# Kernel tuning notes

Measured on AMD Instinct MI355X. Metric: run time of the kernel, lower is better.

## Reference

```python
import jax, jax.numpy as jnp
import numpy as np

N_ELEM = 10   # len(EnvPara.ELEMENTS)
N_ATOMS = 100000
N_DIM = 256


def setup_inputs() -> dict:
    key = jax.random.key(0)
    k = jax.random.split(key, 5)
    return {
        "input_tensor": jax.random.normal(k[0], (N_ATOMS, N_DIM), jnp.float32),
        "species": jax.random.randint(k[1], (N_ATOMS,), 0, N_ELEM, dtype=jnp.int64),
        "W1": jax.random.normal(k[2], (N_ELEM, N_DIM, N_DIM), jnp.float32) / np.sqrt(N_DIM).astype(np.float32),
        "b1": jnp.zeros((N_ELEM, N_DIM), jnp.float32),
        "W2": jax.random.normal(k[3], (N_ELEM, N_DIM, 1), jnp.float32) / np.sqrt(N_DIM).astype(np.float32),
        "b2": jnp.zeros((N_ELEM, 1), jnp.float32),
    }


def _element_linear(x, species, W, b):
    # Species-routed linear: each atom uses the weight/bias of its element.
    # Loop over the small fixed element set (N_ELEM=10) to avoid materializing
    # a [n_atoms, d_in, d_out] gathered-weight tensor.
    out = jnp.zeros((x.shape[0], W.shape[2]), dtype=x.dtype)
    for e in range(W.shape[0]):
        mask = (species == e)[:, None]                      # [n_atoms, 1]
        out = out + jnp.where(mask, x @ W[e] + b[e], jnp.zeros((), x.dtype))
    return out


def reference(input_tensor, species, W1, b1, W2, b2):
    # layer2(silu(layer1(x)))
    h = _element_linear(input_tensor, species, W1, b1)      # [n_atoms, n_dim]
    h = jax.nn.silu(h)                                      # way=0 -> plain SiLU
    return _element_linear(h, species, W2, b2)              # [n_atoms, 1]
```

## Files before the change

kernel.cpp:

```cpp
#include <hip/hip_runtime.h>
#include <hip/hip_bf16.h>
#include <stdint.h>


#define NDIM 256
#define CHUNKS 16
#define BCHUNK 16384
#define TROWS 32
#define ROWB 1040

typedef __attribute__((ext_vector_type(8))) short short8;
typedef __attribute__((ext_vector_type(8))) unsigned short ushort8;
typedef __attribute__((ext_vector_type(4))) float f32x4;

__device__ __forceinline__ unsigned short f2bf(float f) {
  unsigned u = __float_as_uint(f);
  u = (u + 0x7FFFu + ((u >> 16) & 1u)) >> 16;
  return (unsigned short)u;
}

__device__ __forceinline__ void gload_lds16(const void* gsrc, void* ldst) {
  __builtin_amdgcn_global_load_lds(
      (const __attribute__((address_space(1))) unsigned*)gsrc,
      (__attribute__((address_space(3))) unsigned*)(uintptr_t)(unsigned)(uintptr_t)ldst,
      16, 0, 0);
}

__device__ __forceinline__ short8 cvt8(float4 lo, float4 hi) {
  union { short8 s; unsigned u[4]; } r;
  __hip_bfloat162 t;
  t = __float22bfloat162_rn(make_float2(lo.x, lo.y)); r.u[0] = *(unsigned*)&t;
  t = __float22bfloat162_rn(make_float2(lo.z, lo.w)); r.u[1] = *(unsigned*)&t;
  t = __float22bfloat162_rn(make_float2(hi.x, hi.y)); r.u[2] = *(unsigned*)&t;
  t = __float22bfloat162_rn(make_float2(hi.z, hi.w)); r.u[3] = *(unsigned*)&t;
  return r.s;
}


__global__ void convw_k(const float* __restrict__ W1, unsigned short* __restrict__ wt, int NE) {
  int t = blockIdx.x * 256 + threadIdx.x;
  if (t >= NE * 8192) return;
  int n = t & 255;
  int g = (t >> 8) & 3;
  int step = (t >> 10) & 7;
  int e = t >> 13;
  int k0 = step * 32 + g * 8;
  const float* src = W1 + ((size_t)e << 16) + (size_t)k0 * NDIM + n;
  unsigned short v[8];
  #pragma unroll
  for (int j = 0; j < 8; ++j) v[j] = f2bf(src[j * NDIM]);
  char* chunk = (char*)wt + (size_t)(e * 8 + step) * BCHUNK;
  unsigned off = ((unsigned)(n * 64 + g * 16)) ^ ((unsigned)((n & 7) << 4));
  *(ushort8*)(chunk + off) = *(ushort8*)v;
}

__global__ void bhist_k(const int* __restrict__ sp, int n, int* __restrict__ bc, int NE) {
  __shared__ int wc[4][16];
  int tid = threadIdx.x;
  int i = blockIdx.x * 256 + tid;
  int s = (i < n) ? sp[i] : -1;
  int w = tid >> 6, lane = tid & 63;
  for (int e = 0; e < NE; ++e) {
    unsigned long long m = __ballot(s == e);
    if (lane == 0) wc[w][e] = __popcll(m);
  }
  __syncthreads();
  if (tid < NE) bc[blockIdx.x * NE + tid] = wc[0][tid] + wc[1][tid] + wc[2][tid] + wc[3][tid];
}

__global__ void scan_k(const int* __restrict__ bc, int* __restrict__ bo,
                       int* __restrict__ atom_start, int* __restrict__ tile_off,
                       int nblocks, int NE) {
  __shared__ int csum[256];
  __shared__ int coff[256];
  __shared__ int stot[16];
  __shared__ int sbase[16];
  int tid = threadIdx.x;
  int per = (nblocks + CHUNKS - 1) / CHUNKS;
  int e = tid / CHUNKS, c = tid % CHUNKS;
  int b0 = c * per, b1 = b0 + per; if (b1 > nblocks) b1 = nblocks;
  if (tid < NE * CHUNKS) {
    int s = 0;
    for (int b = b0; b < b1; ++b) s += bc[b * NE + e];
    csum[tid] = s;
  }
  __syncthreads();
  if (tid < NE) {
    int r = 0;
    for (int c2 = 0; c2 < CHUNKS; ++c2) { coff[tid * CHUNKS + c2] = r; r += csum[tid * CHUNKS + c2]; }
    stot[tid] = r;
  }
  __syncthreads();
  if (tid == 0) {
    int a = 0, t = 0;
    for (int e2 = 0; e2 < NE; ++e2) {
      sbase[e2] = a;
      atom_start[e2] = a; tile_off[e2] = t;
      a += stot[e2]; t += (stot[e2] + TROWS - 1) / TROWS;
    }
    atom_start[NE] = a; tile_off[NE] = t;
  }
  __syncthreads();
  if (tid < NE * CHUNKS) {
    int run = sbase[e] + coff[tid];
    for (int b = b0; b < b1; ++b) { bo[b * NE + e] = run; run += bc[b * NE + e]; }
  }
}

__global__ void dscatter_k(const int* __restrict__ sp, int n, const int* __restrict__ bo,
                           int* __restrict__ sorted, int NE) {
  __shared__ int wc[4][16];
  int tid = threadIdx.x;
  int i = blockIdx.x * 256 + tid;
  int s = (i < n) ? sp[i] : -1;
  int w = tid >> 6, lane = tid & 63;
  for (int e = 0; e < NE; ++e) {
    unsigned long long m = __ballot(s == e);
    if (lane == 0) wc[w][e] = __popcll(m);
  }
  __syncthreads();
  for (int e = 0; e < NE; ++e) {
    unsigned long long m = __ballot(s == e);
    if (s == e) {
      int wpre = 0;
      for (int w2 = 0; w2 < 4; ++w2) if (w2 < w) wpre += wc[w2][e];
      int rank = __popcll(m & ((1ull << lane) - 1ull));
      sorted[bo[blockIdx.x * NE + e] + wpre + rank] = i;
    }
  }
}


__global__ __launch_bounds__(512, 4) void gemm_k(
    const float* __restrict__ x, const unsigned short* __restrict__ wt,
    const float* __restrict__ b1, const float* __restrict__ w2,
    const float* __restrict__ b2, const int* __restrict__ sorted,
    const int* __restrict__ atom_start, const int* __restrict__ tile_off,
    float* __restrict__ out, int NE)
{
  __shared__ __align__(16) char ldsA[2][TROWS * ROWB];
  __shared__ float partLds[256];
  __shared__ int toffs[17], astart[17];

  int tid = threadIdx.x, lane = tid & 63, wid = tid >> 6;
  int lr = lane & 15, lg = lane >> 4;

  if (tid <= NE) { toffs[tid] = tile_off[tid]; astart[tid] = atom_start[tid]; }
  __syncthreads();

  int ntiles = toffs[NE];
  int nb = gridDim.x, b = blockIdx.x;
  int q = ntiles / nb, rem = ntiles % nb;
  int t0 = b * q + (b < rem ? b : rem);
  int cnt = q + (b < rem ? 1 : 0);
  if (cnt <= 0) return;
  int t1 = t0 + cnt;

  int held_e = -1;
  short8 bf[2][8];
  float bbv[2], wvv[2], b2v = 0.f;

  auto stageA = [&](int t, int buf) {
    int e = 0;
    while (t >= toffs[e + 1]) ++e;
    int rs = astart[e] + (t - toffs[e]) * TROWS;
    int rv = astart[e + 1] - rs; if (rv > TROWS) rv = TROWS;
    #pragma unroll
    for (int i = 0; i < 4; ++i) {
      int rrow = wid * 4 + i;
      int rcl = (rrow < rv) ? rrow : (rv - 1);
      int atom = sorted[rs + rcl];
      gload_lds16(x + (size_t)atom * NDIM + lane * 4, &ldsA[buf][rrow * ROWB]);
    }
  };

  stageA(t0, 0);

  for (int t = t0; t < t1; ++t) {
    int buf = (t - t0) & 1;
    int e = 0;
    while (t >= toffs[e + 1]) ++e;
    int rs = astart[e] + (t - toffs[e]) * TROWS;
    int rv = astart[e + 1] - rs; if (rv > TROWS) rv = TROWS;

    if (e != held_e) {
      held_e = e;
      const char* wbase = (const char*)wt + (size_t)e * 8 * BCHUNK;
      #pragma unroll
      for (int nf = 0; nf < 2; ++nf) {
        int ncol = wid * 32 + nf * 16 + lr;
        unsigned off = ((unsigned)(ncol * 64 + lg * 16)) ^ ((unsigned)((ncol & 7) << 4));
        #pragma unroll
        for (int s = 0; s < 8; ++s)
          bf[nf][s] = *(const short8*)(wbase + (size_t)s * BCHUNK + off);
        bbv[nf] = b1[(size_t)e * NDIM + ncol];
        wvv[nf] = w2[(size_t)e * NDIM + ncol];
      }
      b2v = b2[e];
    }

    __syncthreads();
    if (t + 1 < t1) stageA(t + 1, buf ^ 1);

    f32x4 acc[2][2];
    const f32x4 zero = {0.f, 0.f, 0.f, 0.f};
    #pragma unroll
    for (int i = 0; i < 2; ++i)
      #pragma unroll
      for (int j = 0; j < 2; ++j) acc[i][j] = zero;

    const char* Ab = ldsA[buf];
    #pragma unroll
    for (int step = 0; step < 8; ++step) {
      int k0 = step * 32;
      short8 af[2];
      #pragma unroll
      for (int mf = 0; mf < 2; ++mf) {
        const char* p = Ab + (mf * 16 + lr) * ROWB + (k0 + lg * 8) * 4;
        float4 lo = *(const float4*)p;
        float4 hi = *(const float4*)(p + 16);
        af[mf] = cvt8(lo, hi);
      }
      #pragma unroll
      for (int mf = 0; mf < 2; ++mf)
        #pragma unroll
        for (int nf = 0; nf < 2; ++nf)
          acc[mf][nf] = __builtin_amdgcn_mfma_f32_16x16x32_bf16(af[mf], bf[nf][step], acc[mf][nf], 0, 0, 0);
    }

    float psum[2][4];
    #pragma unroll
    for (int mf = 0; mf < 2; ++mf)
      #pragma unroll
      for (int rg = 0; rg < 4; ++rg) psum[mf][rg] = 0.f;

    #pragma unroll
    for (int nf = 0; nf < 2; ++nf) {
      #pragma unroll
      for (int mf = 0; mf < 2; ++mf)
        #pragma unroll
        for (int rg = 0; rg < 4; ++rg) {
          float h = acc[mf][nf][rg] + bbv[nf];
          float sv = h * __builtin_amdgcn_rcpf(1.f + __expf(-h));
          psum[mf][rg] += sv * wvv[nf];
        }
    }
    #pragma unroll
    for (int mf = 0; mf < 2; ++mf)
      #pragma unroll
      for (int rg = 0; rg < 4; ++rg) {
        float v = psum[mf][rg];
        v += __shfl_xor(v, 1, 64);
        v += __shfl_xor(v, 2, 64);
        v += __shfl_xor(v, 4, 64);
        v += __shfl_xor(v, 8, 64);
        psum[mf][rg] = v;
      }
    if (lr == 0) {
      #pragma unroll
      for (int mf = 0; mf < 2; ++mf)
        #pragma unroll
        for (int rg = 0; rg < 4; ++rg)
          partLds[wid * TROWS + mf * 16 + lg * 4 + rg] = psum[mf][rg];
    }

    asm volatile("s_waitcnt lgkmcnt(0)\n\ts_barrier" ::: "memory");

    if (tid < TROWS && tid < rv) {
      float s = b2v;
      #pragma unroll
      for (int w = 0; w < 8; ++w) s += partLds[w * TROWS + tid];
      out[sorted[rs + tid]] = s;
    }
  }
}


extern "C" void kernel_launch(void* const* d_in, const int* in_sizes, int n_in,
                              void* d_out, int out_size, void* d_ws, size_t ws_size,
                              hipStream_t stream) {
  const float* x  = (const float*)d_in[0];
  const int*   sp = (const int*)d_in[1];
  const float* W1 = (const float*)d_in[2];
  const float* b1 = (const float*)d_in[3];
  const float* W2 = (const float*)d_in[4];
  const float* b2 = (const float*)d_in[5];
  float* out = (float*)d_out;

  int n_atoms = in_sizes[0] / NDIM;
  int NE = in_sizes[2] / (NDIM * NDIM);
  int nblocks = (n_atoms + 255) / 256;

  char* wsb = (char*)d_ws;
  size_t o = 0;
  int* bc = (int*)(wsb + o);         o += ((size_t)nblocks * NE * 4 + 255) & ~(size_t)255;
  int* bo = (int*)(wsb + o);         o += ((size_t)nblocks * NE * 4 + 255) & ~(size_t)255;
  int* atom_start = (int*)(wsb + o); o += 256;
  int* tile_off   = (int*)(wsb + o); o += 256;
  int* sorted     = (int*)(wsb + o); o += ((size_t)n_atoms * 4 + 255) & ~(size_t)255;
  unsigned short* wt = (unsigned short*)(wsb + o);

  hipLaunchKernelGGL(convw_k, dim3((NE * 8192 + 255) / 256), dim3(256), 0, stream,
                     W1, wt, NE);
  hipLaunchKernelGGL(bhist_k, dim3(nblocks), dim3(256), 0, stream, sp, n_atoms, bc, NE);
  hipLaunchKernelGGL(scan_k, dim3(1), dim3(256), 0, stream, bc, bo, atom_start, tile_off,
                     nblocks, NE);
  hipLaunchKernelGGL(dscatter_k, dim3(nblocks), dim3(256), 0, stream, sp, n_atoms, bo,
                     sorted, NE);

  hipLaunchKernelGGL(gemm_k, dim3(512), dim3(512), 0, stream,
                     x, wt, b1, W2, b2, sorted, atom_start, tile_off, out, NE);
}
```

Baseline: 69.83 us.

## Triple-buffer gathered activation tiles and preload atom indices into LDS

The gather pipeline moves from double to triple buffering, so activations are prefetched two tiles ahead, and the full barrier is replaced with explicit vmcnt waits followed by s_barrier. Each block now computes all of its tiles' atom indices into LDS up front, so the per-tile search over `sorted` and its global reads leave the hot loop. The grid is halved to 256 blocks with launch bounds of 2 to make room for the extra LDS buffer. The risks are that hand-tuned vmcnt counts may not match the instructions the compiler actually emits, and that the new MAXT cap silently drops tiles when a block has more than 16.

```diff
diff --git a/kernel.cpp b/kernel.cpp
--- a/kernel.cpp
+++ b/kernel.cpp
@@ -8,6 +8,7 @@
 #define BCHUNK 16384
 #define TROWS 32
 #define ROWB 1040
+#define MAXT 16
 
 typedef __attribute__((ext_vector_type(8))) short short8;
 typedef __attribute__((ext_vector_type(8))) unsigned short ushort8;
@@ -131,15 +132,16 @@
 }
 
 
-__global__ __launch_bounds__(512, 4) void gemm_k(
+__global__ __launch_bounds__(512, 2) void gemm_k(
     const float* __restrict__ x, const unsigned short* __restrict__ wt,
     const float* __restrict__ b1, const float* __restrict__ w2,
     const float* __restrict__ b2, const int* __restrict__ sorted,
     const int* __restrict__ atom_start, const int* __restrict__ tile_off,
     float* __restrict__ out, int NE)
 {
-  __shared__ __align__(16) char ldsA[2][TROWS * ROWB];
+  __shared__ __align__(16) char ldsA[3][TROWS * ROWB];
   __shared__ float partLds[256];
+  __shared__ int ldsAtoms[MAXT * TROWS];
   __shared__ int toffs[17], astart[17];
 
   int tid = threadIdx.x, lane = tid & 63, wid = tid >> 6;
@@ -154,34 +156,43 @@
   int t0 = b * q + (b < rem ? b : rem);
   int cnt = q + (b < rem ? 1 : 0);
   if (cnt <= 0) return;
+  if (cnt > MAXT) cnt = MAXT;
   int t1 = t0 + cnt;
+
+  for (int i = tid; i < cnt * TROWS; i += 512) {
+    int tt = t0 + i / TROWS, r = i % TROWS;
+    int e = 0;
+    while (tt >= toffs[e + 1]) ++e;
+    int rs = astart[e] + (tt - toffs[e]) * TROWS;
+    int rv = astart[e + 1] - rs; if (rv > TROWS) rv = TROWS;
+    ldsAtoms[i] = sorted[rs + (r < rv ? r : rv - 1)];
+  }
+  __syncthreads();
+
+  auto stageA = [&](int t, int buf) {
+    int base = (t - t0) * TROWS;
+    #pragma unroll
+    for (int i = 0; i < 4; ++i) {
+      int rrow = wid * 4 + i;
+      int atom = ldsAtoms[base + rrow];
+      gload_lds16(x + (size_t)atom * NDIM + lane * 4, &ldsA[buf][rrow * ROWB]);
+    }
+  };
 
   int held_e = -1;
   short8 bf[2][8];
   float bbv[2], wvv[2], b2v = 0.f;
 
-  auto stageA = [&](int t, int buf) {
+  stageA(t0, 0);
+  stageA(t0 + 1 < t1 ? t0 + 1 : t1 - 1, 1);
+
+  for (int t = t0; t < t1; ++t) {
+    int buf = (t - t0) % 3;
     int e = 0;
     while (t >= toffs[e + 1]) ++e;
-    int rs = astart[e] + (t - toffs[e]) * TROWS;
-    int rv = astart[e + 1] - rs; if (rv > TROWS) rv = TROWS;
-    #pragma unroll
-    for (int i = 0; i < 4; ++i) {
-      int rrow = wid * 4 + i;
-      int rcl = (rrow < rv) ? rrow : (rv - 1);
-      int atom = sorted[rs + rcl];
-      gload_lds16(x + (size_t)atom * NDIM + lane * 4, &ldsA[buf][rrow * ROWB]);
-    }
-  };
-
-  stageA(t0, 0);
-
-  for (int t = t0; t < t1; ++t) {
-    int buf = (t - t0) & 1;
-    int e = 0;
-    while (t >= toffs[e + 1]) ++e;
-    int rs = astart[e] + (t - toffs[e]) * TROWS;
-    int rv = astart[e + 1] - rs; if (rv > TROWS) rv = TROWS;
+
+    int ts = t + 2 < t1 ? t + 2 : t1 - 1;
+    stageA(ts, (t - t0 + 2) % 3);
 
     if (e != held_e) {
       held_e = e;
@@ -199,8 +210,11 @@
       b2v = b2[e];
     }
 
-    __syncthreads();
-    if (t + 1 < t1) stageA(t + 1, buf ^ 1);
+    if (t == t0)            { asm volatile("s_waitcnt vmcnt(8)" ::: "memory"); }
+    else if (t == t0 + 1)   { asm volatile("s_waitcnt vmcnt(9)" ::: "memory"); }
+    else                    { asm volatile("s_waitcnt vmcnt(10)" ::: "memory"); }
+    __builtin_amdgcn_s_barrier();
+    __builtin_amdgcn_sched_barrier(0);
 
     f32x4 acc[2][2];
     const f32x4 zero = {0.f, 0.f, 0.f, 0.f};
@@ -264,13 +278,15 @@
           partLds[wid * TROWS + mf * 16 + lg * 4 + rg] = psum[mf][rg];
     }
 
-    asm volatile("s_waitcnt lgkmcnt(0)\n\ts_barrier" ::: "memory");
-
-    if (tid < TROWS && tid < rv) {
+    asm volatile("s_waitcnt lgkmcnt(0)" ::: "memory");
+    __builtin_amdgcn_s_barrier();
+    __builtin_amdgcn_sched_barrier(0);
+
+    if (tid < TROWS) {
       float s = b2v;
       #pragma unroll
       for (int w = 0; w < 8; ++w) s += partLds[w * TROWS + tid];
-      out[sorted[rs + tid]] = s;
+      out[ldsAtoms[(t - t0) * TROWS + tid]] = s;
     }
   }
 }
@@ -308,6 +324,6 @@
   hipLaunchKernelGGL(dscatter_k, dim3(nblocks), dim3(256), 0, stream, sp, n_atoms, bo,
                      sorted, NE);
 
-  hipLaunchKernelGGL(gemm_k, dim3(512), dim3(512), 0, stream,
+  hipLaunchKernelGGL(gemm_k, dim3(256), dim3(512), 0, stream,
                      x, wt, b1, W2, b2, sorted, atom_start, tile_off, out, NE);
 }
```

Measured after the change: 74.79 us. 7.1% more time.
